# Kernel optimization log

Hardware: AMD Instinct MI355X
Metric: run time of the kernel (lower is better)

Reference implementation:

```python
import jax, jax.numpy as jnp
from jax import lax
import numpy as np

EPS = 1e-6
B, CIN, HW = 16, 12, 40
E, DEPTH, NH = 768, 12, 12
K, PAD = 10, 5
S = (HW + 2 * PAD - K) // 1 + 1  # 41 (series_len = s0); s1 also 41
L = S * S
HD = E // NH
MLP = 4 * E


def _ln(x, w, b):
    mu = x.mean(-1, keepdims=True)
    xc = x - mu
    var = (xc * xc).mean(-1, keepdims=True)
    return xc * lax.rsqrt(var + EPS) * w + b


def setup_inputs() -> dict:
    key = jax.random.key(0)
    ks = iter(jax.random.split(key, 24))
    r = lambda shape, s=0.02: jax.random.normal(next(ks), shape, jnp.float32) * s
    inp = {
        'x': jax.random.normal(next(ks), (B, CIN, HW, HW), jnp.float32),
        'conv_w': r((E, CIN, K, K)), 'conv_b': jnp.zeros((E,), jnp.float32),
        'pos_embed': r((1, L, E)),
        'ln1_w': jnp.ones((DEPTH, E), jnp.float32), 'ln1_b': jnp.zeros((DEPTH, E), jnp.float32),
        'qkv_w': r((DEPTH, E, 3 * E)), 'qkv_b': jnp.zeros((DEPTH, 3 * E), jnp.float32),
        'proj_w': r((DEPTH, E, E)), 'proj_b': jnp.zeros((DEPTH, E), jnp.float32),
        'ln2_w': jnp.ones((DEPTH, E), jnp.float32), 'ln2_b': jnp.zeros((DEPTH, E), jnp.float32),
        'fc1_w': r((DEPTH, E, MLP)), 'fc1_b': jnp.zeros((DEPTH, MLP), jnp.float32),
        'fc2_w': r((DEPTH, MLP, E)), 'fc2_b': jnp.zeros((DEPTH, E), jnp.float32),
        'lnf_w': jnp.ones((E,), jnp.float32), 'lnf_b': jnp.zeros((E,), jnp.float32),
        'tconv_w': r((E, 1, K, K)), 'tconv_b': jnp.zeros((1,), jnp.float32),
    }
    return inp


def reference(x, conv_w, conv_b, pos_embed, ln1_w, ln1_b, qkv_w, qkv_b,
              proj_w, proj_b, ln2_w, ln2_b, fc1_w, fc1_b, fc2_w, fc2_b,
              lnf_w, lnf_b, tconv_w, tconv_b):
    scale = HD ** -0.5
    # patch embed: Conv2d -> (B, E, 41, 41) -> flatten -> (B, L, E)
    h = lax.conv_general_dilated(x, conv_w, (1, 1), [(PAD, PAD), (PAD, PAD)])
    h = h + conv_b[None, :, None, None]
    t = h.reshape(B, E, L).transpose(0, 2, 1) + pos_embed

    for i in range(DEPTH):
        # attention over each of the S series slices (N = S tokens each), batched
        y = _ln(t, ln1_w[i], ln1_b[i])
        qkv = (y @ qkv_w[i] + qkv_b[i]).reshape(B, S, S, 3, NH, HD)
        q, k, v = qkv[:, :, :, 0], qkv[:, :, :, 1], qkv[:, :, :, 2]  # (B,S,N,NH,HD)
        attn = jnp.einsum('bsnhd,bsmhd->bshnm', q, k) * scale
        attn = jax.nn.softmax(attn, axis=-1)
        o = jnp.einsum('bshnm,bsmhd->bsnhd', attn, v).reshape(B, L, E)
        t = t + (o @ proj_w[i] + proj_b[i])
        # MLP
        z = _ln(t, ln2_w[i], ln2_b[i])
        z = jax.nn.gelu(z @ fc1_w[i] + fc1_b[i], approximate=False)
        t = t + (z @ fc2_w[i] + fc2_b[i])

    t = _ln(t, lnf_w, lnf_b)
    feat = t.reshape(B, S, S, E).transpose(0, 3, 1, 2)  # (B, E, 41, 41)
    # ConvTranspose2d(k=10, s=1, p=5) == direct conv with flipped/swapped kernel, pad k-1-p=4
    wt = jnp.flip(tconv_w, (2, 3)).transpose(1, 0, 2, 3)  # (out_c, E, K, K)
    out = lax.conv_general_dilated(feat, wt, (1, 1), [(K - 1 - PAD,) * 2] * 2)
    out = out + tconv_b[None, :, None, None]
    return jnp.squeeze(out)  # (B, 40, 40)
```

## Files before the change

### kernel.cpp

```cpp
#include <hip/hip_runtime.h>
#include <cstdint>

typedef __bf16 bf16_t;
typedef __attribute__((ext_vector_type(8))) __bf16 bf16x8;
typedef __attribute__((ext_vector_type(4))) __bf16 bf16x4;
typedef __attribute__((ext_vector_type(4))) float f32x4;

#define TOKENS 26896
#define LLEN   1681
#define SDIM   41
#define EDIM   768

__device__ __forceinline__ void gload_lds16(const bf16_t* g, bf16_t* l) {
  auto gp = reinterpret_cast<const __attribute__((address_space(1))) char*>(
      reinterpret_cast<uintptr_t>(g));
  auto lp = reinterpret_cast<__attribute__((address_space(3))) char*>(
      reinterpret_cast<uintptr_t>(l));
  __builtin_amdgcn_global_load_lds(gp, lp, 16, 0, 0);
}

enum { EPI_T_POS = 0, EPI_BF16 = 1, EPI_ADD_T = 2, EPI_GELU = 3, EPI_F32 = 4 };

template <int EPI>
__global__ __launch_bounds__(256, 3) void gemm4_kernel(
    const bf16_t* __restrict__ A, const bf16_t* __restrict__ Bt,
    const float* __restrict__ bias, float* __restrict__ fout,
    bf16_t* __restrict__ bout, const float* __restrict__ pos,
    int M, int N, int K, int ntn, int nwg, int mtiles)
{
  __shared__ bf16_t lds[3 * 8192];
  const int tid = threadIdx.x, wave = tid >> 6, lane = tid & 63;
  const int wr = wave >> 1, wc = wave & 1;

  int id = blockIdx.x;
  {
    const int q = nwg >> 3, r = nwg & 7;
    const int xcd = id & 7, ix = id >> 3;
    id = (xcd < r ? xcd * (q + 1) : r * (q + 1) + (xcd - r) * q) + ix;
  }
  const int gsz = mtiles * 6;
  const int cg  = id / gsz, rem = id % gsz;
  const int row0 = (rem / 6) * 128;
  const int col0 = (cg * 6 + rem % 6) * 128;
  const int NT = K >> 5;

  const int srow = tid >> 2;
  const int sswz = ((tid & 3) ^ ((srow >> 1) & 3)) * 8;
  const bf16_t* aptr[2];
  const bf16_t* bptr[2];
  #pragma unroll
  for (int p = 0; p < 2; ++p) {
    int ar = row0 + p * 64 + srow; if (ar > M - 1) ar = M - 1;
    int br = col0 + p * 64 + srow; if (br > N - 1) br = N - 1;
    aptr[p] = A  + (size_t)ar * K + sswz;
    bptr[p] = Bt + (size_t)br * K + sswz;
  }
  bf16_t* sdst = lds + tid * 8;

  #define STAGE(BUF, KT) do {                                   \
    const int koff_ = (KT) << 5;                                \
    gload_lds16(aptr[0] + koff_, sdst + (BUF)*8192);            \
    gload_lds16(aptr[1] + koff_, sdst + (BUF)*8192 + 2048);     \
    gload_lds16(bptr[0] + koff_, sdst + (BUF)*8192 + 4096);     \
    gload_lds16(bptr[1] + koff_, sdst + (BUF)*8192 + 6144);     \
  } while (0)

  const int l15 = lane & 15, l4 = lane >> 4;
  const int fswz = (l4 ^ ((l15 >> 1) & 3)) << 3;
  const bf16_t* lA = lds + (wr * 64 + l15) * 32 + fswz;
  const bf16_t* lB = lds + 4096 + (wc * 64 + l15) * 32 + fswz;

  f32x4 acc[4][4] = {};

  #define COMPUTE(BUF) do {                                     \
    bf16x8 fa[4], fb[4];                                        \
    _Pragma("unroll")                                           \
    for (int m_ = 0; m_ < 4; ++m_) fa[m_] = *(const bf16x8*)(lA + (BUF)*8192 + m_*512); \
    _Pragma("unroll")                                           \
    for (int n_ = 0; n_ < 4; ++n_) fb[n_] = *(const bf16x8*)(lB + (BUF)*8192 + n_*512); \
    _Pragma("unroll")                                           \
    for (int m_ = 0; m_ < 4; ++m_)                              \
      _Pragma("unroll")                                         \
      for (int n_ = 0; n_ < 4; ++n_)                            \
        acc[m_][n_] = __builtin_amdgcn_mfma_f32_16x16x32_bf16(fa[m_], fb[n_], acc[m_][n_], 0, 0, 0); \
  } while (0)

  #define STEP(SC, SN, T) do {                                  \
    if ((T) + 2 < NT) STAGE(SN, (T) + 2);                       \
    COMPUTE(SC);                                                \
    if ((T) + 2 < NT)      asm volatile("s_waitcnt vmcnt(4)" ::: "memory"); \
    else if ((T) + 1 < NT) asm volatile("s_waitcnt vmcnt(0)" ::: "memory"); \
    __builtin_amdgcn_s_barrier();                               \
    __builtin_amdgcn_sched_barrier(0);                          \
  } while (0)

  STAGE(0, 0);
  if (NT > 1) {
    STAGE(1, 1);
    asm volatile("s_waitcnt vmcnt(4)" ::: "memory");
  } else {
    asm volatile("s_waitcnt vmcnt(0)" ::: "memory");
  }
  __builtin_amdgcn_s_barrier();
  __builtin_amdgcn_sched_barrier(0);

  for (int kt = 0; kt < NT; kt += 3) {
    STEP(0, 2, kt);
    if (kt + 1 < NT) STEP(1, 0, kt + 1);
    if (kt + 2 < NT) STEP(2, 1, kt + 2);
  }
  #undef STEP
  #undef STAGE
  #undef COMPUTE

  const int rgrp = lane >> 4;
  #pragma unroll
  for (int m = 0; m < 4; ++m) {
    #pragma unroll
    for (int n = 0; n < 4; ++n) {
      const int col = col0 + wc * 64 + n * 16 + l15;
      if (col >= N) continue;
      const int rbase = row0 + wr * 64 + m * 16 + rgrp * 4;
      float bv = 0.f;
      if constexpr (EPI != EPI_F32) bv = bias[col];
      #pragma unroll
      for (int r = 0; r < 4; ++r) {
        const int rr = rbase + r;
        if (rr >= M) continue;
        const float v = acc[m][n][r] + bv;
        const size_t o = (size_t)rr * N + col;
        if constexpr (EPI == EPI_T_POS) {
          const int l = rr % LLEN;
          bout[o] = (bf16_t)(v + pos[(size_t)l * N + col]);
        } else if constexpr (EPI == EPI_BF16) {
          bout[o] = (bf16_t)v;
        } else if constexpr (EPI == EPI_ADD_T) {
          bout[o] = (bf16_t)((float)bout[o] + v);
        } else if constexpr (EPI == EPI_GELU) {
          const float u = v + 0.044715f * v * v * v;
          const float gg = v / (1.f + __expf(-1.5957691216f * u));
          bout[o] = (bf16_t)gg;
        } else {
          fout[o] = v;
        }
      }
    }
  }
}

__global__ __launch_bounds__(256) void gemm128_f32(
    const bf16_t* __restrict__ A, const bf16_t* __restrict__ Bt,
    float* __restrict__ fout, int M, int N, int K)
{
  __shared__ bf16_t As[128 * 32];
  __shared__ bf16_t Bs[128 * 32];
  const int tid = threadIdx.x, wave = tid >> 6, lane = tid & 63;
  const int row0 = blockIdx.x * 128, col0 = blockIdx.y * 128;
  const int wr = wave >> 1, wc = wave & 1;
  f32x4 acc[4][4] = {};
  const int srow = lane >> 2, skoff = (lane & 3) * 8;
  const int nsteps = K >> 5;
  for (int kt = 0; kt < nsteps; ++kt) {
    const int k0 = kt << 5;
    #pragma unroll
    for (int i = 0; i < 2; ++i) {
      const int r = (i * 4 + wave) * 16 + srow;
      int arow = row0 + r; if (arow > M - 1) arow = M - 1;
      int brow = col0 + r; if (brow > N - 1) brow = N - 1;
      gload_lds16(A  + (size_t)arow * K + k0 + skoff, &As[r * 32 + skoff]);
      gload_lds16(Bt + (size_t)brow * K + k0 + skoff, &Bs[r * 32 + skoff]);
    }
    asm volatile("s_waitcnt vmcnt(0)" ::: "memory");
    __syncthreads();
    const int lrow = lane & 15, lk = (lane >> 4) * 8;
    bf16x8 af[4], bfr[4];
    #pragma unroll
    for (int mi = 0; mi < 4; ++mi)
      af[mi] = *(const bf16x8*)&As[(wr * 64 + mi * 16 + lrow) * 32 + lk];
    #pragma unroll
    for (int ni = 0; ni < 4; ++ni)
      bfr[ni] = *(const bf16x8*)&Bs[(wc * 64 + ni * 16 + lrow) * 32 + lk];
    #pragma unroll
    for (int mi = 0; mi < 4; ++mi)
      #pragma unroll
      for (int ni = 0; ni < 4; ++ni)
        acc[mi][ni] = __builtin_amdgcn_mfma_f32_16x16x32_bf16(af[mi], bfr[ni], acc[mi][ni], 0, 0, 0);
    __syncthreads();
  }
  const int lcol = lane & 15, rgrp = lane >> 4;
  #pragma unroll
  for (int mi = 0; mi < 4; ++mi)
    #pragma unroll
    for (int ni = 0; ni < 4; ++ni) {
      const int col = col0 + wc * 64 + ni * 16 + lcol;
      if (col >= N) continue;
      const int rbase = row0 + wr * 64 + mi * 16 + rgrp * 4;
      #pragma unroll
      for (int r = 0; r < 4; ++r) {
        const int rr = rbase + r;
        if (rr >= M) continue;
        fout[(size_t)rr * N + col] = acc[mi][ni][r];
      }
    }
}

__global__ __launch_bounds__(256) void ln_kernel(
    const bf16_t* __restrict__ t, const float* __restrict__ w,
    const float* __restrict__ b, bf16_t* __restrict__ y)
{
  const int token = blockIdx.x * 4 + (threadIdx.x >> 6);
  const int lane  = threadIdx.x & 63;
  const bf16_t* xp = t + (size_t)token * EDIM;
  const bf16x8 a8 = *(const bf16x8*)(xp + lane * 8);
  const bf16x4 a4 = *(const bf16x4*)(xp + 512 + lane * 4);
  float va[12];
  #pragma unroll
  for (int j = 0; j < 8; ++j) va[j] = (float)a8[j];
  #pragma unroll
  for (int j = 0; j < 4; ++j) va[8 + j] = (float)a4[j];
  float s = 0.f;
  #pragma unroll
  for (int j = 0; j < 12; ++j) s += va[j];
  #pragma unroll
  for (int off = 32; off; off >>= 1) s += __shfl_xor(s, off);
  const float mu = s * (1.f / 768.f);
  float q = 0.f;
  #pragma unroll
  for (int j = 0; j < 12; ++j) { const float d = va[j] - mu; q += d * d; }
  #pragma unroll
  for (int off = 32; off; off >>= 1) q += __shfl_xor(q, off);
  const float rs = rsqrtf(q * (1.f / 768.f) + 1e-6f);

  bf16_t* yp = y + (size_t)token * EDIM;
  {
    const int e0 = lane * 8;
    const float4 w0 = ((const float4*)(w + e0))[0];
    const float4 w1 = ((const float4*)(w + e0))[1];
    const float4 b0 = ((const float4*)(b + e0))[0];
    const float4 b1 = ((const float4*)(b + e0))[1];
    bf16x8 o;
    o[0] = (bf16_t)((va[0] - mu) * rs * w0.x + b0.x);
    o[1] = (bf16_t)((va[1] - mu) * rs * w0.y + b0.y);
    o[2] = (bf16_t)((va[2] - mu) * rs * w0.z + b0.z);
    o[3] = (bf16_t)((va[3] - mu) * rs * w0.w + b0.w);
    o[4] = (bf16_t)((va[4] - mu) * rs * w1.x + b1.x);
    o[5] = (bf16_t)((va[5] - mu) * rs * w1.y + b1.y);
    o[6] = (bf16_t)((va[6] - mu) * rs * w1.z + b1.z);
    o[7] = (bf16_t)((va[7] - mu) * rs * w1.w + b1.w);
    *(bf16x8*)(yp + e0) = o;
  }
  {
    const int e0 = 512 + lane * 4;
    const float4 w0 = *(const float4*)(w + e0);
    const float4 b0 = *(const float4*)(b + e0);
    bf16x4 o;
    o[0] = (bf16_t)((va[8]  - mu) * rs * w0.x + b0.x);
    o[1] = (bf16_t)((va[9]  - mu) * rs * w0.y + b0.y);
    o[2] = (bf16_t)((va[10] - mu) * rs * w0.z + b0.z);
    o[3] = (bf16_t)((va[11] - mu) * rs * w0.w + b0.w);
    *(bf16x4*)(yp + e0) = o;
  }
}

__global__ __launch_bounds__(256) void attn_kernel(
    const bf16_t* __restrict__ qkv, bf16_t* __restrict__ o)
{
  const int blk = blockIdx.x;
  const int h  = blk % 12;
  const int bs = blk / 12;
  const int s1 = bs % SDIM;
  const int b  = bs / SDIM;
  __shared__ float Qs[SDIM][65], Ks[SDIM][65], Vs[SDIM][65], Ps[SDIM][44];
  const int tid = threadIdx.x;
  const size_t base = ((size_t)b * LLEN + (size_t)s1 * SDIM);

  for (int idx = tid; idx < SDIM * 8; idx += 256) {
    const int m = idx >> 3, c = idx & 7;
    const bf16_t* p = qkv + (base + m) * 2304 + h * 64 + c * 8;
    const bf16x8 qv = *(const bf16x8*)(p);
    const bf16x8 kv = *(const bf16x8*)(p + 768);
    const bf16x8 vv = *(const bf16x8*)(p + 1536);
    #pragma unroll
    for (int j = 0; j < 8; ++j) {
      Qs[m][c * 8 + j] = (float)qv[j];
      Ks[m][c * 8 + j] = (float)kv[j];
      Vs[m][c * 8 + j] = (float)vv[j];
    }
  }
  __syncthreads();

  for (int idx = tid; idx < SDIM * SDIM; idx += 256) {
    const int n = idx / SDIM, m = idx % SDIM;
    float s = 0.f;
    #pragma unroll
    for (int d = 0; d < 64; ++d) s += Qs[n][d] * Ks[m][d];
    Ps[n][m] = s * 0.125f;
  }
  __syncthreads();

  {
    const int row = tid >> 2, sub = tid & 3;
    if (row < SDIM) {
      float mx = -1e30f;
      for (int m = sub; m < SDIM; m += 4) mx = fmaxf(mx, Ps[row][m]);
      mx = fmaxf(mx, __shfl_xor(mx, 1));
      mx = fmaxf(mx, __shfl_xor(mx, 2));
      float sum = 0.f;
      for (int m = sub; m < SDIM; m += 4) {
        const float e = __expf(Ps[row][m] - mx);
        Ps[row][m] = e;
        sum += e;
      }
      sum += __shfl_xor(sum, 1);
      sum += __shfl_xor(sum, 2);
      const float inv = 1.f / sum;
      for (int m = sub; m < SDIM; m += 4) Ps[row][m] *= inv;
    }
  }
  __syncthreads();

  for (int idx = tid; idx < SDIM * 64; idx += 256) {
    const int n = idx >> 6, d = idx & 63;
    float s = 0.f;
    #pragma unroll
    for (int m = 0; m < SDIM; ++m) s += Ps[n][m] * Vs[m][d];
    o[(base + n) * EDIM + h * 64 + d] = (bf16_t)s;
  }
}

__global__ __launch_bounds__(256) void transpose_kernel(
    const float* __restrict__ in, bf16_t* __restrict__ out, int K, int N)
{
  __shared__ float tile[32][33];
  const int k0 = blockIdx.x * 32, n0 = blockIdx.y * 32;
  const int tx = threadIdx.x & 31, ty = threadIdx.x >> 5;
  #pragma unroll
  for (int i = 0; i < 32; i += 8) {
    const int k = k0 + ty + i, n = n0 + tx;
    if (k < K && n < N) tile[ty + i][tx] = in[(size_t)k * N + n];
  }
  __syncthreads();
  #pragma unroll
  for (int i = 0; i < 32; i += 8) {
    const int n = n0 + ty + i, k = k0 + tx;
    if (n < N && k < K) out[(size_t)n * K + k] = (bf16_t)tile[tx][ty + i];
  }
}

__global__ __launch_bounds__(256) void im2col_kernel(
    const float* __restrict__ x, bf16_t* __restrict__ col, int tok0, int ntok)
{
  const size_t idx = (size_t)blockIdx.x * 256 + threadIdx.x;
  if (idx >= (size_t)ntok * 1216) return;
  const int kk = (int)(idx % 1216);
  const size_t tok = tok0 + idx / 1216;
  const int b = (int)(tok / LLEN), l = (int)(tok % LLEN);
  const int s1 = l / SDIM, s2 = l % SDIM;
  float v = 0.f;
  if (kk < 1200) {
    const int cin = kk / 100, r = kk % 100, ky = r / 10, kx = r % 10;
    const int iy = s1 - 5 + ky, ix = s2 - 5 + kx;
    if (iy >= 0 && iy < 40 && ix >= 0 && ix < 40)
      v = x[((size_t)(b * 12 + cin) * 40 + iy) * 40 + ix];
  }
  col[idx] = (bf16_t)v;
}

__global__ __launch_bounds__(256) void convw_kernel(
    const float* __restrict__ w, bf16_t* __restrict__ out)
{
  const int idx = blockIdx.x * 256 + threadIdx.x;
  const int kk = idx % 1216, e = idx / 1216;
  const float v = (kk < 1200) ? w[(size_t)e * 1200 + kk] : 0.f;
  out[idx] = (bf16_t)v;
}

__global__ __launch_bounds__(256) void tconvw_kernel(
    const float* __restrict__ w, bf16_t* __restrict__ out)
{
  const int idx = blockIdx.x * 256 + threadIdx.x;
  const int e = idx % 768, tap = idx / 768;
  const int ky = tap / 10, kx = tap % 10;
  out[idx] = (bf16_t)w[(size_t)e * 100 + (9 - ky) * 10 + (9 - kx)];
}

__global__ __launch_bounds__(256) void outconv_kernel(
    const float* __restrict__ g, const float* __restrict__ tb,
    float* __restrict__ out)
{
  const int idx = blockIdx.x * 256 + threadIdx.x;
  if (idx >= 16 * 40 * 40) return;
  const int x = idx % 40, y = (idx / 40) % 40, b = idx / 1600;
  float s = tb[0];
  #pragma unroll
  for (int ky = 0; ky < 10; ++ky) {
    const int ty_ = y - 4 + ky;
    if (ty_ < 0 || ty_ >= SDIM) continue;
    #pragma unroll
    for (int kx = 0; kx < 10; ++kx) {
      const int tx_ = x - 4 + kx;
      if (tx_ < 0 || tx_ >= SDIM) continue;
      s += g[((size_t)b * LLEN + ty_ * SDIM + tx_) * 100 + ky * 10 + kx];
    }
  }
  out[idx] = s;
}

extern "C" void kernel_launch(void* const* d_in, const int* in_sizes, int n_in,
                              void* d_out, int out_size, void* d_ws, size_t ws_size,
                              hipStream_t stream)
{
  const float* x       = (const float*)d_in[0];
  const float* conv_w  = (const float*)d_in[1];
  const float* conv_b  = (const float*)d_in[2];
  const float* pos     = (const float*)d_in[3];
  const float* ln1_w   = (const float*)d_in[4];
  const float* ln1_b   = (const float*)d_in[5];
  const float* qkv_w   = (const float*)d_in[6];
  const float* qkv_b   = (const float*)d_in[7];
  const float* proj_w  = (const float*)d_in[8];
  const float* proj_b  = (const float*)d_in[9];
  const float* ln2_w   = (const float*)d_in[10];
  const float* ln2_b   = (const float*)d_in[11];
  const float* fc1_w   = (const float*)d_in[12];
  const float* fc1_b   = (const float*)d_in[13];
  const float* fc2_w   = (const float*)d_in[14];
  const float* fc2_b   = (const float*)d_in[15];
  const float* lnf_w   = (const float*)d_in[16];
  const float* lnf_b   = (const float*)d_in[17];
  const float* tconv_w = (const float*)d_in[18];
  const float* tconv_b = (const float*)d_in[19];
  float* out = (float*)d_out;

  const int nch = (ws_size >= 262200000UL) ? 1
                : (ws_size >= 179500000UL) ? 2 : 4;
  const int cht = TOKENS / nch;

  char* p = (char*)d_ws;
  auto alloc = [&](size_t bytes) {
    char* r = p;
    p += (bytes + 255) & ~(size_t)255;
    return r;
  };
  bf16_t* wbuf = (bf16_t*)alloc((size_t)768 * 9216 * 2);
  bf16_t* t    = (bf16_t*)alloc((size_t)TOKENS * EDIM * 2);
  bf16_t* ybuf = (bf16_t*)alloc((size_t)TOKENS * EDIM * 2);
  bf16_t* hbuf = (bf16_t*)alloc((size_t)cht * 3072 * 2);

  bf16_t* Wq = wbuf;
  bf16_t* Wp = Wq + (size_t)2304 * 768;
  bf16_t* W1 = Wp + (size_t)768 * 768;
  bf16_t* W2 = W1 + (size_t)3072 * 768;

  auto g4 = [&](int epi, const bf16_t* A, const bf16_t* Bt,
                const float* bias, bf16_t* bo, const float* pe,
                int M, int N, int K) {
    const int mtiles = (M + 127) / 128;
    const int ntn = N / 128;
    const int nwg = mtiles * ntn;
    switch (epi) {
      case EPI_T_POS: gemm4_kernel<EPI_T_POS><<<nwg, 256, 0, stream>>>(A, Bt, bias, nullptr, bo, pe, M, N, K, ntn, nwg, mtiles); break;
      case EPI_BF16:  gemm4_kernel<EPI_BF16 ><<<nwg, 256, 0, stream>>>(A, Bt, bias, nullptr, bo, pe, M, N, K, ntn, nwg, mtiles); break;
      case EPI_ADD_T: gemm4_kernel<EPI_ADD_T><<<nwg, 256, 0, stream>>>(A, Bt, bias, nullptr, bo, pe, M, N, K, ntn, nwg, mtiles); break;
      default:        gemm4_kernel<EPI_GELU ><<<nwg, 256, 0, stream>>>(A, Bt, bias, nullptr, bo, pe, M, N, K, ntn, nwg, mtiles); break;
    }
  };

  convw_kernel<<<(768 * 1216) / 256, 256, 0, stream>>>(conv_w, wbuf);
  for (int c = 0; c < nch; ++c) {
    const int tok0 = c * cht;
    im2col_kernel<<<(unsigned)(((size_t)cht * 1216 + 255) / 256), 256, 0, stream>>>(x, hbuf, tok0, cht);
    g4(EPI_T_POS, hbuf, wbuf, conv_b, t + (size_t)tok0 * EDIM, pos, cht, EDIM, 1216);
  }

  for (int i = 0; i < 12; ++i) {
    transpose_kernel<<<dim3(24, 72), 256, 0, stream>>>(qkv_w + (size_t)i * 768 * 2304, Wq, 768, 2304);
    transpose_kernel<<<dim3(24, 24), 256, 0, stream>>>(proj_w + (size_t)i * 768 * 768, Wp, 768, 768);
    transpose_kernel<<<dim3(24, 96), 256, 0, stream>>>(fc1_w + (size_t)i * 768 * 3072, W1, 768, 3072);
    transpose_kernel<<<dim3(96, 24), 256, 0, stream>>>(fc2_w + (size_t)i * 3072 * 768, W2, 3072, 768);

    ln_kernel<<<TOKENS / 4, 256, 0, stream>>>(t, ln1_w + i * EDIM, ln1_b + i * EDIM, ybuf);
    for (int c = 0; c < nch; ++c) {
      const size_t ro = (size_t)c * cht;
      g4(EPI_BF16, ybuf + ro * EDIM, Wq, qkv_b + i * 2304, hbuf, nullptr, cht, 2304, 768);
      attn_kernel<<<(16 / nch) * SDIM * 12, 256, 0, stream>>>(hbuf, ybuf + ro * EDIM);
    }
    g4(EPI_ADD_T, ybuf, Wp, proj_b + i * EDIM, t, nullptr, TOKENS, EDIM, 768);

    ln_kernel<<<TOKENS / 4, 256, 0, stream>>>(t, ln2_w + i * EDIM, ln2_b + i * EDIM, ybuf);
    for (int c = 0; c < nch; ++c) {
      const size_t ro = (size_t)c * cht;
      g4(EPI_GELU, ybuf + ro * EDIM, W1, fc1_b + i * 3072, hbuf, nullptr, cht, 3072, 768);
      g4(EPI_ADD_T, hbuf, W2, fc2_b + i * EDIM, t + ro * EDIM, nullptr, cht, EDIM, 3072);
    }
  }

  ln_kernel<<<TOKENS / 4, 256, 0, stream>>>(t, lnf_w, lnf_b, ybuf);
  tconvw_kernel<<<(100 * 768) / 256, 256, 0, stream>>>(tconv_w, wbuf);
  gemm128_f32<<<dim3((TOKENS + 127) / 128, 1), 256, 0, stream>>>(ybuf, wbuf, (float*)hbuf, TOKENS, 100, 768);
  outconv_kernel<<<100, 256, 0, stream>>>((const float*)hbuf, tconv_b, out);
}
```

Baseline: 9.774 ms.

## Add 256x256-tile 8-wave GEMM with fine-grained phased pipelining for large GEMMs

Adds a new GEMM kernel with 512 threads, 256x256 output tiles, a K-step of 64 and 128KB of dynamic LDS. Each k-step is split into phases that interleave the global-to-LDS loads with MFMA groups, using barriers and setprio to raise compute priority. QKV, FC1, FC2 and the patch-embed GEMMs now use it, while the projection GEMM stays on the old 128x128 kernel. The conv K is padded from 1216 to 1280 so it divides by 128. The larger tiles are meant to raise data reuse per LDS load, at the cost of one workgroup per CU, fewer tiles (worse wave quantization) and a requirement that K be a multiple of 128.

After: 11.06 ms. 13.2% more time.

```diff
diff --git a/kernel.cpp b/kernel.cpp
--- a/kernel.cpp
+++ b/kernel.cpp
@@ -22,15 +22,15 @@
 enum { EPI_T_POS = 0, EPI_BF16 = 1, EPI_ADD_T = 2, EPI_GELU = 3, EPI_F32 = 4 };
 
 template <int EPI>
-__global__ __launch_bounds__(256, 3) void gemm4_kernel(
+__global__ __launch_bounds__(512, 1) void gemm8p_kernel(
     const bf16_t* __restrict__ A, const bf16_t* __restrict__ Bt,
-    const float* __restrict__ bias, float* __restrict__ fout,
-    bf16_t* __restrict__ bout, const float* __restrict__ pos,
+    const float* __restrict__ bias, bf16_t* __restrict__ bout,
+    const float* __restrict__ pos,
     int M, int N, int K, int ntn, int nwg, int mtiles)
 {
-  __shared__ bf16_t lds[3 * 8192];
+  extern __shared__ bf16_t lds[];
   const int tid = threadIdx.x, wave = tid >> 6, lane = tid & 63;
-  const int wr = wave >> 1, wc = wave & 1;
+  const int wr = wave >> 2, wc = wave & 3;
 
   int id = blockIdx.x;
   {
@@ -38,91 +38,136 @@
     const int xcd = id & 7, ix = id >> 3;
     id = (xcd < r ? xcd * (q + 1) : r * (q + 1) + (xcd - r) * q) + ix;
   }
-  const int gsz = mtiles * 6;
-  const int cg  = id / gsz, rem = id % gsz;
-  const int row0 = (rem / 6) * 128;
-  const int col0 = (cg * 6 + rem % 6) * 128;
-  const int NT = K >> 5;
-
-  const int srow = tid >> 2;
-  const int sswz = ((tid & 3) ^ ((srow >> 1) & 3)) * 8;
-  const bf16_t* aptr[2];
-  const bf16_t* bptr[2];
-  #pragma unroll
-  for (int p = 0; p < 2; ++p) {
-    int ar = row0 + p * 64 + srow; if (ar > M - 1) ar = M - 1;
-    int br = col0 + p * 64 + srow; if (br > N - 1) br = N - 1;
-    aptr[p] = A  + (size_t)ar * K + sswz;
-    bptr[p] = Bt + (size_t)br * K + sswz;
-  }
+  const int gsz = mtiles * 3;
+  const int cg = id / gsz, rem = id % gsz;
+  const int row0 = (rem / 3) * 256;
+  const int col0 = (cg * 3 + rem % 3) * 256;
+  const int NT  = K >> 6;
+  const int NIT = NT >> 1;
+
+  const int srow = tid >> 3;
+  const int scol = (((tid & 7) ^ (srow & 7)) << 3);
+  const bf16_t* pA[2][2];
+  const bf16_t* pB[2][2];
+  #pragma unroll
+  for (int h = 0; h < 2; ++h)
+    #pragma unroll
+    for (int p = 0; p < 2; ++p) {
+      int ar = row0 + h * 128 + p * 64 + srow; if (ar > M - 1) ar = M - 1;
+      int br = col0 + h * 128 + p * 64 + srow; if (br > N - 1) br = N - 1;
+      pA[h][p] = A  + (size_t)ar * K + scol;
+      pB[h][p] = Bt + (size_t)br * K + scol;
+    }
   bf16_t* sdst = lds + tid * 8;
 
-  #define STAGE(BUF, KT) do {                                   \
-    const int koff_ = (KT) << 5;                                \
-    gload_lds16(aptr[0] + koff_, sdst + (BUF)*8192);            \
-    gload_lds16(aptr[1] + koff_, sdst + (BUF)*8192 + 2048);     \
-    gload_lds16(bptr[0] + koff_, sdst + (BUF)*8192 + 4096);     \
-    gload_lds16(bptr[1] + koff_, sdst + (BUF)*8192 + 6144);     \
+  #define STA(D, H, KOFF) do {                                              \
+    gload_lds16(pA[H][0] + (KOFF), sdst + (D)*32768 + (H)*8192);            \
+    gload_lds16(pA[H][1] + (KOFF), sdst + (D)*32768 + (H)*8192 + 4096);     \
   } while (0)
+  #define STB(D, H, KOFF) do {                                              \
+    gload_lds16(pB[H][0] + (KOFF), sdst + (D)*32768 + 16384 + (H)*8192);    \
+    gload_lds16(pB[H][1] + (KOFF), sdst + (D)*32768 + 16384 + (H)*8192 + 4096); \
+  } while (0)
 
   const int l15 = lane & 15, l4 = lane >> 4;
-  const int fswz = (l4 ^ ((l15 >> 1) & 3)) << 3;
-  const bf16_t* lA = lds + (wr * 64 + l15) * 32 + fswz;
-  const bf16_t* lB = lds + 4096 + (wc * 64 + l15) * 32 + fswz;
-
-  f32x4 acc[4][4] = {};
-
-  #define COMPUTE(BUF) do {                                     \
-    bf16x8 fa[4], fb[4];                                        \
-    _Pragma("unroll")                                           \
-    for (int m_ = 0; m_ < 4; ++m_) fa[m_] = *(const bf16x8*)(lA + (BUF)*8192 + m_*512); \
-    _Pragma("unroll")                                           \
-    for (int n_ = 0; n_ < 4; ++n_) fb[n_] = *(const bf16x8*)(lB + (BUF)*8192 + n_*512); \
-    _Pragma("unroll")                                           \
-    for (int m_ = 0; m_ < 4; ++m_)                              \
-      _Pragma("unroll")                                         \
-      for (int n_ = 0; n_ < 4; ++n_)                            \
-        acc[m_][n_] = __builtin_amdgcn_mfma_f32_16x16x32_bf16(fa[m_], fb[n_], acc[m_][n_], 0, 0, 0); \
+  const int ck0 = ((l4    ) ^ (l15 & 7)) << 3;
+  const int ck1 = ((l4 + 4) ^ (l15 & 7)) << 3;
+  const bf16_t* lA0 = lds + (wr * 128 + l15) * 64 + ck0;
+  const bf16_t* lA1 = lds + (wr * 128 + l15) * 64 + ck1;
+  const bf16_t* lB0 = lds + 16384 + (wc * 64 + l15) * 64 + ck0;
+  const bf16_t* lB1 = lds + 16384 + (wc * 64 + l15) * 64 + ck1;
+
+  f32x4 acc[8][4] = {};
+  bf16x8 fb0[4], fb1[4];
+
+  #define LOADFB(D) do {                                                    \
+    _Pragma("unroll")                                                       \
+    for (int n_ = 0; n_ < 4; ++n_) {                                        \
+      fb0[n_] = *(const bf16x8*)(lB0 + (D)*32768 + n_*1024);                \
+      fb1[n_] = *(const bf16x8*)(lB1 + (D)*32768 + n_*1024);                \
+    }                                                                       \
   } while (0)
 
-  #define STEP(SC, SN, T) do {                                  \
-    if ((T) + 2 < NT) STAGE(SN, (T) + 2);                       \
-    COMPUTE(SC);                                                \
-    if ((T) + 2 < NT)      asm volatile("s_waitcnt vmcnt(4)" ::: "memory"); \
-    else if ((T) + 1 < NT) asm volatile("s_waitcnt vmcnt(0)" ::: "memory"); \
-    __builtin_amdgcn_s_barrier();                               \
-    __builtin_amdgcn_sched_barrier(0);                          \
+  #define VM4  asm volatile("s_waitcnt vmcnt(4)" ::: "memory")
+  #define VM0  asm volatile("s_waitcnt vmcnt(0)" ::: "memory")
+  #define NOP_ ((void)0)
+
+  #define PHASE(D, MS, STG, VM) do {                                        \
+    bf16x8 fa00 = *(const bf16x8*)(lA0 + (D)*32768 + (MS)*1024);            \
+    bf16x8 fa01 = *(const bf16x8*)(lA1 + (D)*32768 + (MS)*1024);            \
+    bf16x8 fa10 = *(const bf16x8*)(lA0 + (D)*32768 + ((MS)+1)*1024);        \
+    bf16x8 fa11 = *(const bf16x8*)(lA1 + (D)*32768 + ((MS)+1)*1024);        \
+    STG;                                                                    \
+    __builtin_amdgcn_s_barrier();                                           \
+    asm volatile("s_waitcnt lgkmcnt(0)" ::: "memory");                      \
+    __builtin_amdgcn_sched_barrier(0);                                      \
+    __builtin_amdgcn_s_setprio(1);                                          \
+    _Pragma("unroll")                                                       \
+    for (int n_ = 0; n_ < 4; ++n_)                                          \
+      acc[MS][n_] = __builtin_amdgcn_mfma_f32_16x16x32_bf16(fa00, fb0[n_], acc[MS][n_], 0, 0, 0); \
+    _Pragma("unroll")                                                       \
+    for (int n_ = 0; n_ < 4; ++n_)                                          \
+      acc[MS][n_] = __builtin_amdgcn_mfma_f32_16x16x32_bf16(fa01, fb1[n_], acc[MS][n_], 0, 0, 0); \
+    _Pragma("unroll")                                                       \
+    for (int n_ = 0; n_ < 4; ++n_)                                          \
+      acc[(MS)+1][n_] = __builtin_amdgcn_mfma_f32_16x16x32_bf16(fa10, fb0[n_], acc[(MS)+1][n_], 0, 0, 0); \
+    _Pragma("unroll")                                                       \
+    for (int n_ = 0; n_ < 4; ++n_)                                          \
+      acc[(MS)+1][n_] = __builtin_amdgcn_mfma_f32_16x16x32_bf16(fa11, fb1[n_], acc[(MS)+1][n_], 0, 0, 0); \
+    __builtin_amdgcn_s_setprio(0);                                          \
+    VM;                                                                     \
+    __builtin_amdgcn_s_barrier();                                           \
   } while (0)
 
-  STAGE(0, 0);
-  if (NT > 1) {
-    STAGE(1, 1);
-    asm volatile("s_waitcnt vmcnt(4)" ::: "memory");
-  } else {
-    asm volatile("s_waitcnt vmcnt(0)" ::: "memory");
-  }
+  STA(0, 0, 0); STA(0, 1, 0);
+  STB(0, 0, 0); STB(0, 1, 0);
+  STB(1, 0, 64); STB(1, 1, 64);
+  VM4;
   __builtin_amdgcn_s_barrier();
   __builtin_amdgcn_sched_barrier(0);
 
-  for (int kt = 0; kt < NT; kt += 3) {
-    STEP(0, 2, kt);
-    if (kt + 1 < NT) STEP(1, 0, kt + 1);
-    if (kt + 2 < NT) STEP(2, 1, kt + 2);
-  }
-  #undef STEP
-  #undef STAGE
-  #undef COMPUTE
+  int kb = 0;
+  for (int it = 0; it < NIT - 1; ++it) {
+    LOADFB(0);
+    PHASE(0, 0, STA(1, 0, kb + 64),  NOP_);
+    PHASE(0, 2, STA(1, 1, kb + 64),  NOP_);
+    PHASE(0, 4, STB(0, 0, kb + 128), NOP_);
+    PHASE(0, 6, STB(0, 1, kb + 128), VM4);
+    LOADFB(1);
+    PHASE(1, 0, STA(0, 0, kb + 128), NOP_);
+    PHASE(1, 2, STA(0, 1, kb + 128), NOP_);
+    PHASE(1, 4, STB(1, 0, kb + 192), NOP_);
+    PHASE(1, 6, STB(1, 1, kb + 192), VM4);
+    kb += 128;
+  }
+  LOADFB(0);
+  PHASE(0, 0, STA(1, 0, kb + 64), NOP_);
+  PHASE(0, 2, STA(1, 1, kb + 64), NOP_);
+  PHASE(0, 4, NOP_, NOP_);
+  PHASE(0, 6, NOP_, VM0);
+  LOADFB(1);
+  PHASE(1, 0, NOP_, NOP_);
+  PHASE(1, 2, NOP_, NOP_);
+  PHASE(1, 4, NOP_, NOP_);
+  PHASE(1, 6, NOP_, NOP_);
+
+  #undef PHASE
+  #undef LOADFB
+  #undef STA
+  #undef STB
+  #undef VM4
+  #undef VM0
+  #undef NOP_
 
   const int rgrp = lane >> 4;
   #pragma unroll
-  for (int m = 0; m < 4; ++m) {
+  for (int m = 0; m < 8; ++m) {
     #pragma unroll
     for (int n = 0; n < 4; ++n) {
       const int col = col0 + wc * 64 + n * 16 + l15;
       if (col >= N) continue;
-      const int rbase = row0 + wr * 64 + m * 16 + rgrp * 4;
-      float bv = 0.f;
-      if constexpr (EPI != EPI_F32) bv = bias[col];
+      const int rbase = row0 + wr * 128 + m * 16 + rgrp * 4;
+      const float bv = bias[col];
       #pragma unroll
       for (int r = 0; r < 4; ++r) {
         const int rr = rbase + r;
@@ -136,12 +181,125 @@
           bout[o] = (bf16_t)v;
         } else if constexpr (EPI == EPI_ADD_T) {
           bout[o] = (bf16_t)((float)bout[o] + v);
-        } else if constexpr (EPI == EPI_GELU) {
+        } else {
           const float u = v + 0.044715f * v * v * v;
-          const float gg = v / (1.f + __expf(-1.5957691216f * u));
-          bout[o] = (bf16_t)gg;
+          bout[o] = (bf16_t)(v / (1.f + __expf(-1.5957691216f * u)));
+        }
+      }
+    }
+  }
+}
+
+template <int EPI>
+__global__ __launch_bounds__(256, 3) void gemm4_kernel(
+    const bf16_t* __restrict__ A, const bf16_t* __restrict__ Bt,
+    const float* __restrict__ bias, bf16_t* __restrict__ bout,
+    int M, int N, int K, int ntn, int nwg, int mtiles)
+{
+  __shared__ bf16_t lds[3 * 8192];
+  const int tid = threadIdx.x, wave = tid >> 6, lane = tid & 63;
+  const int wr = wave >> 1, wc = wave & 1;
+
+  int id = blockIdx.x;
+  {
+    const int q = nwg >> 3, r = nwg & 7;
+    const int xcd = id & 7, ix = id >> 3;
+    id = (xcd < r ? xcd * (q + 1) : r * (q + 1) + (xcd - r) * q) + ix;
+  }
+  const int gsz = mtiles * 6;
+  const int cg  = id / gsz, rem = id % gsz;
+  const int row0 = (rem / 6) * 128;
+  const int col0 = (cg * 6 + rem % 6) * 128;
+  const int NT = K >> 5;
+
+  const int srow = tid >> 2;
+  const int sswz = ((tid & 3) ^ ((srow >> 1) & 3)) * 8;
+  const bf16_t* aptr[2];
+  const bf16_t* bptr[2];
+  #pragma unroll
+  for (int p = 0; p < 2; ++p) {
+    int ar = row0 + p * 64 + srow; if (ar > M - 1) ar = M - 1;
+    int br = col0 + p * 64 + srow; if (br > N - 1) br = N - 1;
+    aptr[p] = A  + (size_t)ar * K + sswz;
+    bptr[p] = Bt + (size_t)br * K + sswz;
+  }
+  bf16_t* sdst = lds + tid * 8;
+
+  #define STAGE(BUF, KT) do {                                   \
+    const int koff_ = (KT) << 5;                                \
+    gload_lds16(aptr[0] + koff_, sdst + (BUF)*8192);            \
+    gload_lds16(aptr[1] + koff_, sdst + (BUF)*8192 + 2048);     \
+    gload_lds16(bptr[0] + koff_, sdst + (BUF)*8192 + 4096);     \
+    gload_lds16(bptr[1] + koff_, sdst + (BUF)*8192 + 6144);     \
+  } while (0)
+
+  const int l15 = lane & 15, l4 = lane >> 4;
+  const int fswz = (l4 ^ ((l15 >> 1) & 3)) << 3;
+  const bf16_t* lA = lds + (wr * 64 + l15) * 32 + fswz;
+  const bf16_t* lB = lds + 4096 + (wc * 64 + l15) * 32 + fswz;
+
+  f32x4 acc[4][4] = {};
+
+  #define COMPUTE(BUF) do {                                     \
+    bf16x8 fa[4], fb[4];                                        \
+    _Pragma("unroll")                                           \
+    for (int m_ = 0; m_ < 4; ++m_) fa[m_] = *(const bf16x8*)(lA + (BUF)*8192 + m_*512); \
+    _Pragma("unroll")                                           \
+    for (int n_ = 0; n_ < 4; ++n_) fb[n_] = *(const bf16x8*)(lB + (BUF)*8192 + n_*512); \
+    _Pragma("unroll")                                           \
+    for (int m_ = 0; m_ < 4; ++m_)                              \
+      _Pragma("unroll")                                         \
+      for (int n_ = 0; n_ < 4; ++n_)                            \
+        acc[m_][n_] = __builtin_amdgcn_mfma_f32_16x16x32_bf16(fa[m_], fb[n_], acc[m_][n_], 0, 0, 0); \
+  } while (0)
+
+  #define STEP(SC, SN, T) do {                                  \
+    if ((T) + 2 < NT) STAGE(SN, (T) + 2);                       \
+    COMPUTE(SC);                                                \
+    if ((T) + 2 < NT)      asm volatile("s_waitcnt vmcnt(4)" ::: "memory"); \
+    else if ((T) + 1 < NT) asm volatile("s_waitcnt vmcnt(0)" ::: "memory"); \
+    __builtin_amdgcn_s_barrier();                               \
+    __builtin_amdgcn_sched_barrier(0);                          \
+  } while (0)
+
+  STAGE(0, 0);
+  if (NT > 1) {
+    STAGE(1, 1);
+    asm volatile("s_waitcnt vmcnt(4)" ::: "memory");
+  } else {
+    asm volatile("s_waitcnt vmcnt(0)" ::: "memory");
+  }
+  __builtin_amdgcn_s_barrier();
+  __builtin_amdgcn_sched_barrier(0);
+
+  for (int kt = 0; kt < NT; kt += 3) {
+    STEP(0, 2, kt);
+    if (kt + 1 < NT) STEP(1, 0, kt + 1);
+    if (kt + 2 < NT) STEP(2, 1, kt + 2);
+  }
+  #undef STEP
+  #undef STAGE
+  #undef COMPUTE
+
+  const int rgrp = lane >> 4;
+  #pragma unroll
+  for (int m = 0; m < 4; ++m) {
+    #pragma unroll
+    for (int n = 0; n < 4; ++n) {
+      const int col = col0 + wc * 64 + n * 16 + l15;
+      if (col >= N) continue;
+      const int rbase = row0 + wr * 64 + m * 16 + rgrp * 4;
+      const float bv = bias[col];
+      #pragma unroll
+      for (int r = 0; r < 4; ++r) {
+        const int rr = rbase + r;
+        if (rr >= M) continue;
+        const float v = acc[m][n][r] + bv;
+        const size_t o = (size_t)rr * N + col;
+        if constexpr (EPI == EPI_ADD_T) {
+          bout[o] = (bf16_t)((float)bout[o] + v);
         } else {
-          fout[o] = v;
+          bout[o] = (bf16_t)v;
         }
       }
     }
@@ -351,9 +509,9 @@
     const float* __restrict__ x, bf16_t* __restrict__ col, int tok0, int ntok)
 {
   const size_t idx = (size_t)blockIdx.x * 256 + threadIdx.x;
-  if (idx >= (size_t)ntok * 1216) return;
-  const int kk = (int)(idx % 1216);
-  const size_t tok = tok0 + idx / 1216;
+  if (idx >= (size_t)ntok * 1280) return;
+  const int kk = (int)(idx % 1280);
+  const size_t tok = tok0 + idx / 1280;
   const int b = (int)(tok / LLEN), l = (int)(tok % LLEN);
   const int s1 = l / SDIM, s2 = l % SDIM;
   float v = 0.f;
@@ -370,7 +528,7 @@
     const float* __restrict__ w, bf16_t* __restrict__ out)
 {
   const int idx = blockIdx.x * 256 + threadIdx.x;
-  const int kk = idx % 1216, e = idx / 1216;
+  const int kk = idx % 1280, e = idx / 1280;
   const float v = (kk < 1200) ? w[(size_t)e * 1200 + kk] : 0.f;
   out[idx] = (bf16_t)v;
 }
@@ -432,6 +590,12 @@
   const float* tconv_b = (const float*)d_in[19];
   float* out = (float*)d_out;
 
+  constexpr int LDS8P = 131072;
+  hipFuncSetAttribute((const void*)gemm8p_kernel<EPI_T_POS>, hipFuncAttributeMaxDynamicSharedMemorySize, LDS8P);
+  hipFuncSetAttribute((const void*)gemm8p_kernel<EPI_BF16 >, hipFuncAttributeMaxDynamicSharedMemorySize, LDS8P);
+  hipFuncSetAttribute((const void*)gemm8p_kernel<EPI_ADD_T>, hipFuncAttributeMaxDynamicSharedMemorySize, LDS8P);
+  hipFuncSetAttribute((const void*)gemm8p_kernel<EPI_GELU >, hipFuncAttributeMaxDynamicSharedMemorySize, LDS8P);
+
   const int nch = (ws_size >= 262200000UL) ? 1
                 : (ws_size >= 179500000UL) ? 2 : 4;
   const int cht = TOKENS / nch;
@@ -452,25 +616,32 @@
   bf16_t* W1 = Wp + (size_t)768 * 768;
   bf16_t* W2 = W1 + (size_t)3072 * 768;
 
-  auto g4 = [&](int epi, const bf16_t* A, const bf16_t* Bt,
-                const float* bias, bf16_t* bo, const float* pe,
-                int M, int N, int K) {
+  auto g8p = [&](int epi, const bf16_t* A, const bf16_t* Bt,
+                 const float* bias, bf16_t* bo, const float* pe,
+                 int M, int N, int K) {
+    const int mtiles = (M + 255) / 256;
+    const int ntn = N / 256;
+    const int nwg = mtiles * ntn;
+    switch (epi) {
+      case EPI_T_POS: gemm8p_kernel<EPI_T_POS><<<nwg, 512, LDS8P, stream>>>(A, Bt, bias, bo, pe, M, N, K, ntn, nwg, mtiles); break;
+      case EPI_BF16:  gemm8p_kernel<EPI_BF16 ><<<nwg, 512, LDS8P, stream>>>(A, Bt, bias, bo, pe, M, N, K, ntn, nwg, mtiles); break;
+      case EPI_ADD_T: gemm8p_kernel<EPI_ADD_T><<<nwg, 512, LDS8P, stream>>>(A, Bt, bias, bo, pe, M, N, K, ntn, nwg, mtiles); break;
+      default:        gemm8p_kernel<EPI_GELU ><<<nwg, 512, LDS8P, stream>>>(A, Bt, bias, bo, pe, M, N, K, ntn, nwg, mtiles); break;
+    }
+  };
+  auto g4 = [&](const bf16_t* A, const bf16_t* Bt, const float* bias,
+                bf16_t* bo, int M, int N, int K) {
     const int mtiles = (M + 127) / 128;
     const int ntn = N / 128;
     const int nwg = mtiles * ntn;
-    switch (epi) {
-      case EPI_T_POS: gemm4_kernel<EPI_T_POS><<<nwg, 256, 0, stream>>>(A, Bt, bias, nullptr, bo, pe, M, N, K, ntn, nwg, mtiles); break;
-      case EPI_BF16:  gemm4_kernel<EPI_BF16 ><<<nwg, 256, 0, stream>>>(A, Bt, bias, nullptr, bo, pe, M, N, K, ntn, nwg, mtiles); break;
-      case EPI_ADD_T: gemm4_kernel<EPI_ADD_T><<<nwg, 256, 0, stream>>>(A, Bt, bias, nullptr, bo, pe, M, N, K, ntn, nwg, mtiles); break;
-      default:        gemm4_kernel<EPI_GELU ><<<nwg, 256, 0, stream>>>(A, Bt, bias, nullptr, bo, pe, M, N, K, ntn, nwg, mtiles); break;
-    }
+    gemm4_kernel<EPI_ADD_T><<<nwg, 256, 0, stream>>>(A, Bt, bias, bo, M, N, K, ntn, nwg, mtiles);
   };
 
-  convw_kernel<<<(768 * 1216) / 256, 256, 0, stream>>>(conv_w, wbuf);
+  convw_kernel<<<(768 * 1280) / 256, 256, 0, stream>>>(conv_w, wbuf);
   for (int c = 0; c < nch; ++c) {
     const int tok0 = c * cht;
-    im2col_kernel<<<(unsigned)(((size_t)cht * 1216 + 255) / 256), 256, 0, stream>>>(x, hbuf, tok0, cht);
-    g4(EPI_T_POS, hbuf, wbuf, conv_b, t + (size_t)tok0 * EDIM, pos, cht, EDIM, 1216);
+    im2col_kernel<<<(unsigned)(((size_t)cht * 1280 + 255) / 256), 256, 0, stream>>>(x, hbuf, tok0, cht);
+    g8p(EPI_T_POS, hbuf, wbuf, conv_b, t + (size_t)tok0 * EDIM, pos, cht, EDIM, 1280);
   }
 
   for (int i = 0; i < 12; ++i) {
@@ -482,16 +653,16 @@
     ln_kernel<<<TOKENS / 4, 256, 0, stream>>>(t, ln1_w + i * EDIM, ln1_b + i * EDIM, ybuf);
     for (int c = 0; c < nch; ++c) {
       const size_t ro = (size_t)c * cht;
-      g4(EPI_BF16, ybuf + ro * EDIM, Wq, qkv_b + i * 2304, hbuf, nullptr, cht, 2304, 768);
+      g8p(EPI_BF16, ybuf + ro * EDIM, Wq, qkv_b + i * 2304, hbuf, nullptr, cht, 2304, 768);
       attn_kernel<<<(16 / nch) * SDIM * 12, 256, 0, stream>>>(hbuf, ybuf + ro * EDIM);
     }
-    g4(EPI_ADD_T, ybuf, Wp, proj_b + i * EDIM, t, nullptr, TOKENS, EDIM, 768);
+    g4(ybuf, Wp, proj_b + i * EDIM, t, TOKENS, EDIM, 768);
 
     ln_kernel<<<TOKENS / 4, 256, 0, stream>>>(t, ln2_w + i * EDIM, ln2_b + i * EDIM, ybuf);
     for (int c = 0; c < nch; ++c) {
       const size_t ro = (size_t)c * cht;
-      g4(EPI_GELU, ybuf + ro * EDIM, W1, fc1_b + i * 3072, hbuf, nullptr, cht, 3072, 768);
-      g4(EPI_ADD_T, hbuf, W2, fc2_b + i * EDIM, t + ro * EDIM, nullptr, cht, EDIM, 3072);
+      g8p(EPI_GELU, ybuf + ro * EDIM, W1, fc1_b + i * 3072, hbuf, nullptr, cht, 3072, 768);
+      g8p(EPI_ADD_T, hbuf, W2, fc2_b + i * EDIM, t + ro * EDIM, nullptr, cht, EDIM, 3072);
     }
   }
 
```
